# Performance work log

Hardware: AMD Instinct MI355X
Metric: run time of the kernel (lower is better)

## Reference

```python
import jax, jax.numpy as jnp
import numpy as np

WEIGHT_BITS = 8
INPUT_BITS = 8


def fake_quant(t, bits):
    """Per-tensor symmetric absmax fake quantization with straight-through estimator."""
    qmax = 2.0 ** (bits - 1) - 1.0  # e.g. 127 for 8 bits
    scale = jnp.maximum(jnp.max(jnp.abs(t)), 1e-8) / qmax
    q = jnp.round(t / scale) * scale
    return t + jax.lax.stop_gradient(q - t)


def setup_inputs() -> dict:
    key = jax.random.key(0)
    k0, k1, k2, k3 = jax.random.split(key, 4)
    d, f, n = 4096, 11008, 4096
    s_in = 1.0 / np.sqrt(d)
    s_ff = 1.0 / np.sqrt(f)
    return {
        "x": jax.random.normal(k0, (n, d), jnp.float32),
        "w1": jax.random.normal(k1, (f, d), jnp.float32) * s_in,  # fc1: embed -> ffn
        "w3": jax.random.normal(k2, (f, d), jnp.float32) * s_in,  # fc3: gate proj
        "w2": jax.random.normal(k3, (d, f), jnp.float32) * s_ff,  # fc2: ffn -> embed
    }


def reference(x, w1, w3, w2):
    # quantized fc3 -> silu gate
    xq = fake_quant(x, INPUT_BITS)
    gate = jax.nn.silu(jnp.einsum('nd,fd->nf', xq, fake_quant(w3, WEIGHT_BITS)))
    # quantized fc1, multiplied by gate (GLU)
    h = jnp.einsum('nd,fd->nf', xq, fake_quant(w1, WEIGHT_BITS)) * gate
    # subln=False -> no ffn_layernorm; dropout=0 (eval)
    hq = fake_quant(h, INPUT_BITS)
    out = jnp.einsum('nf,df->nd', hq, fake_quant(w2, WEIGHT_BITS))
    return out
```

## Files before the change

### kernel.cpp

```cpp
#include <hip/hip_runtime.h>
#include <hip/hip_bf16.h>

typedef __attribute__((ext_vector_type(4))) int int4v;

#define MFMA_I8(a, b, c) __builtin_amdgcn_mfma_i32_16x16x64_i8((a), (b), (c), 0, 0, 0)
#define GLDS16(g, l)                                                                        \
  __builtin_amdgcn_global_load_lds((const __attribute__((address_space(1))) void*)(g),      \
                                   (__attribute__((address_space(3))) void*)(l), 16, 0, 0)
#define SBAR() __builtin_amdgcn_s_barrier()
#define SCHED0() __builtin_amdgcn_sched_barrier(0)

static constexpr int NTOK = 4096;
static constexpr int DDIM = 4096;
static constexpr int FDIM = 11008;


__device__ __forceinline__ float wave_max64(float m) {
#pragma unroll
  for (int o = 32; o > 0; o >>= 1) m = fmaxf(m, __shfl_xor(m, o));
  return m;
}

__global__ void zero_slots(unsigned* s) {
  if (threadIdx.x < 16) s[threadIdx.x] = 0u;
}

__device__ __forceinline__ void absmax_body(const float* __restrict__ p, int n4,
                                            unsigned* __restrict__ slot) {
  float m = 0.f;
  const int stride = gridDim.x * blockDim.x;
  for (int i = blockIdx.x * blockDim.x + threadIdx.x; i < n4; i += stride) {
    float4 v = reinterpret_cast<const float4*>(p)[i];
    m = fmaxf(fmaxf(fabsf(v.x), fabsf(v.y)), fmaxf(fmaxf(fabsf(v.z), fabsf(v.w)), m));
  }
  m = wave_max64(m);
  __shared__ float wm[4];
  const int lane = threadIdx.x & 63, w = threadIdx.x >> 6;
  if (lane == 0) wm[w] = m;
  __syncthreads();
  if (threadIdx.x == 0) {
    m = fmaxf(fmaxf(wm[0], wm[1]), fmaxf(wm[2], wm[3]));
    atomicMax(slot, __float_as_uint(m));
  }
}

__global__ void absmax4(const float* x, const float* w1, const float* w3, const float* w2,
                        unsigned* slots, int n4x, int n4w) {
  const int seg = blockIdx.y;
  const float* p = (seg == 0) ? x : (seg == 1) ? w1 : (seg == 2) ? w3 : w2;
  absmax_body(p, seg == 0 ? n4x : n4w, slots + seg);
}

__device__ __forceinline__ void quant_body(const float* __restrict__ in,
                                           unsigned* __restrict__ out, int n4,
                                           const unsigned* __restrict__ slot) {
  const float s = fmaxf(__uint_as_float(*slot), 1e-8f) / 127.0f;
  const int stride = gridDim.x * blockDim.x;
  for (int i = blockIdx.x * blockDim.x + threadIdx.x; i < n4; i += stride) {
    float4 v = reinterpret_cast<const float4*>(in)[i];
    const int q0 = (int)rintf(v.x / s), q1 = (int)rintf(v.y / s);
    const int q2 = (int)rintf(v.z / s), q3 = (int)rintf(v.w / s);
    out[i] = (unsigned)(q0 & 255) | ((unsigned)(q1 & 255) << 8) |
             ((unsigned)(q2 & 255) << 16) | ((unsigned)(q3 & 255) << 24);
  }
}

__device__ __forceinline__ void quantW_frag_body(const float* __restrict__ in,
                                                 int4v* __restrict__ out,
                                                 const unsigned* __restrict__ slot) {
  const float s = fmaxf(__uint_as_float(*slot), 1e-8f) / 127.0f;
  const int total = FDIM * (DDIM / 16);
  const int stride = gridDim.x * blockDim.x;
  for (int u = blockIdx.x * blockDim.x + threadIdx.x; u < total; u += stride) {
    const int block = u >> 8;
    const int sidx = u & 255;
    const int fi = sidx >> 6;
    const int l = sidx & 63;
    const int p = block >> 5;
    const int kt = block & 31;
    const int f = p * 32 + (fi & 1) * 16 + (l & 15);
    const int k0 = kt * 128 + (fi >> 1) * 64 + (l >> 4) * 16;
    const float4* src = reinterpret_cast<const float4*>(in + (size_t)f * DDIM + k0);
    unsigned r[4];
#pragma unroll
    for (int j = 0; j < 4; ++j) {
      float4 v = src[j];
      const int q0 = (int)rintf(v.x / s), q1 = (int)rintf(v.y / s);
      const int q2 = (int)rintf(v.z / s), q3 = (int)rintf(v.w / s);
      r[j] = (unsigned)(q0 & 255) | ((unsigned)(q1 & 255) << 8) |
             ((unsigned)(q2 & 255) << 16) | ((unsigned)(q3 & 255) << 24);
    }
    out[u] = (int4v){(int)r[0], (int)r[1], (int)r[2], (int)r[3]};
  }
}

__global__ void quant4(const float* x, const float* w1, const float* w3, const float* w2,
                       unsigned* qx, unsigned* qw1, unsigned* qw3, unsigned* qw2,
                       const unsigned* slots, int n4x, int n4w) {
  const int seg = blockIdx.y;
  if (seg == 0) quant_body(x, qx, n4x, slots + 0);
  else if (seg == 1) quantW_frag_body(w1, (int4v*)qw1, slots + 1);
  else if (seg == 2) quantW_frag_body(w3, (int4v*)qw3, slots + 2);
  else quant_body(w2, qw2, n4w, slots + 3);
}

__global__ void quant_kernel(const float* __restrict__ in, unsigned* __restrict__ out,
                             int n4, const unsigned* __restrict__ slot) {
  quant_body(in, out, n4, slot);
}

__global__ __launch_bounds__(512, 2) void gemm_glu(
    const signed char* __restrict__ Aq, const signed char* __restrict__ B3f,
    const signed char* __restrict__ B1f, float* __restrict__ H,
    const unsigned* __restrict__ slots, unsigned* __restrict__ hslot) {
  constexpr int K = DDIM;
  constexpr int NT = K >> 7;
  __shared__ char lds[32768];

  const int t = threadIdx.x;
  const int l = t & 63;
  const int w = t >> 6;

  const int gx = gridDim.x, gy = gridDim.y;
  const int nwg = gx * gy;
  const int i0 = blockIdx.y * gx + blockIdx.x;
  const int cid = (i0 & 7) * (nwg >> 3) + (i0 >> 3);
  const int rowA0 = (cid % gy) << 7;
  const int colB0 = (cid / gy) << 8;

  const int rlA = t >> 3;
  const int glA = (t & 7) ^ (rlA & 7);
  const signed char* aP = Aq + (size_t)(rowA0 + rlA) * K + glA * 16;
  const size_t r64 = (size_t)64 * K;
  const int stW = w * 1024;

  const int p0 = (colB0 >> 5) + w;
  const signed char* w3b = B3f + (size_t)p0 * 32 * 4096 + l * 16;
  const signed char* w1b = B1f + (size_t)p0 * 32 * 4096 + l * 16;

#define STAGE_A(KT, BUF)                               \
  do {                                                 \
    const size_t kO_ = (size_t)(KT) * 128;             \
    GLDS16(aP + kO_, &lds[(BUF) + stW]);               \
    GLDS16(aP + r64 + kO_, &lds[(BUF) + 8192 + stW]);  \
  } while (0)

#define LDSF(BASE, R, G)                                                      \
  (*reinterpret_cast<const int4v*>(                                           \
      &lds[(BASE) + (R)*128 + (((G) ^ ((R)&7)) << 4)]))

  int4v acc3[8][2], acc1[8][2];
#pragma unroll
  for (int m = 0; m < 8; ++m)
#pragma unroll
    for (int n = 0; n < 2; ++n) {
      acc3[m][n] = (int4v){0, 0, 0, 0};
      acc1[m][n] = (int4v){0, 0, 0, 0};
    }

  const int lr = l & 15;
  const int cr = l >> 4;

  int4v b3k0[2], b3k1[2], b1k0[2], b1k1[2];

  STAGE_A(0, 0);
  {
    const signed char* p3_ = w3b;
    const signed char* p1_ = w1b;
    b3k0[0] = *(const int4v*)(p3_);
    b3k0[1] = *(const int4v*)(p3_ + 1024);
    b3k1[0] = *(const int4v*)(p3_ + 2048);
    b3k1[1] = *(const int4v*)(p3_ + 3072);
    b1k0[0] = *(const int4v*)(p1_);
    b1k0[1] = *(const int4v*)(p1_ + 1024);
    b1k1[0] = *(const int4v*)(p1_ + 2048);
    b1k1[1] = *(const int4v*)(p1_ + 3072);
  }

  for (int kt = 0; kt < NT; ++kt) {
    const int rb = (kt & 1) * 16384;
    const bool nx = (kt + 1 < NT);
    const signed char* p3n = w3b + (size_t)(kt + 1) * 4096;
    const signed char* p1n = w1b + (size_t)(kt + 1) * 4096;

    SCHED0();
    asm volatile("s_waitcnt vmcnt(8)" ::: "memory");
    SBAR();
    SCHED0();

    if (nx) STAGE_A(kt + 1, rb ^ 16384);

    int4v a_[8];
#pragma unroll
    for (int m = 0; m < 8; ++m) a_[m] = LDSF(rb, m * 16 + lr, cr);
    __builtin_amdgcn_s_setprio(1);
#pragma unroll
    for (int m = 0; m < 8; ++m) {
      acc3[m][0] = MFMA_I8(a_[m], b3k0[0], acc3[m][0]);
      acc3[m][1] = MFMA_I8(a_[m], b3k0[1], acc3[m][1]);
      acc1[m][0] = MFMA_I8(a_[m], b1k0[0], acc1[m][0]);
      acc1[m][1] = MFMA_I8(a_[m], b1k0[1], acc1[m][1]);
    }
    __builtin_amdgcn_s_setprio(0);

    if (nx) {
      b3k0[0] = *(const int4v*)(p3n);
      b3k0[1] = *(const int4v*)(p3n + 1024);
      b1k0[0] = *(const int4v*)(p1n);
      b1k0[1] = *(const int4v*)(p1n + 1024);
    }

#pragma unroll
    for (int m = 0; m < 8; ++m) a_[m] = LDSF(rb, m * 16 + lr, 4 + cr);
    __builtin_amdgcn_s_setprio(1);
#pragma unroll
    for (int m = 0; m < 8; ++m) {
      acc3[m][0] = MFMA_I8(a_[m], b3k1[0], acc3[m][0]);
      acc3[m][1] = MFMA_I8(a_[m], b3k1[1], acc3[m][1]);
      acc1[m][0] = MFMA_I8(a_[m], b1k1[0], acc1[m][0]);
      acc1[m][1] = MFMA_I8(a_[m], b1k1[1], acc1[m][1]);
    }
    __builtin_amdgcn_s_setprio(0);

    if (nx) {
      b3k1[0] = *(const int4v*)(p3n + 2048);
      b3k1[1] = *(const int4v*)(p3n + 3072);
      b1k1[0] = *(const int4v*)(p1n + 2048);
      b1k1[1] = *(const int4v*)(p1n + 3072);
    }
  }

  const float sx = fmaxf(__uint_as_float(slots[0]), 1e-8f) / 127.0f;
  const float sw1 = fmaxf(__uint_as_float(slots[1]), 1e-8f) / 127.0f;
  const float sw3 = fmaxf(__uint_as_float(slots[2]), 1e-8f) / 127.0f;
  const float s3 = sx * sw3, s1 = sx * sw1;
  const int crow0 = rowA0 + ((l >> 4) << 2);
  const int ccol0 = colB0 + w * 32 + lr;
  float hmax = 0.f;
#pragma unroll
  for (int m = 0; m < 8; ++m)
#pragma unroll
    for (int n = 0; n < 2; ++n)
#pragma unroll
      for (int j = 0; j < 4; ++j) {
        const int row = crow0 + m * 16 + j;
        const int col = ccol0 + n * 16;
        const float g = (float)acc3[m][n][j] * s3;
        const float gate = g / (1.f + expf(-g));
        const float h = (float)acc1[m][n][j] * s1 * gate;
        H[(size_t)row * FDIM + col] = h;
        hmax = fmaxf(hmax, fabsf(h));
      }
  hmax = wave_max64(hmax);
  if (l == 0) atomicMax(hslot, __float_as_uint(hmax));
#undef STAGE_A
#undef LDSF
}

__global__ __launch_bounds__(512, 2) void gemm_down(
    const signed char* __restrict__ Aq, const signed char* __restrict__ Bq,
    float* __restrict__ C, const unsigned* __restrict__ slots, int sA, int sB,
    int K, int ldc) {
  __shared__ char lds[131072];

  const int t = threadIdx.x;
  const int l = t & 63;
  const int w = t >> 6;
  const int wm = w >> 2;
  const int wn = w & 3;

  const int gx = gridDim.x, gy = gridDim.y;
  const int nwg = gx * gy;
  const int i0 = blockIdx.y * gx + blockIdx.x;
  const int cid = (i0 & 7) * (nwg >> 3) + (i0 >> 3);
  const int rowA0 = (cid % gy) << 8;
  const int colB0 = (cid / gy) << 8;

  const int rl = t >> 3;
  const int gl = (t & 7) ^ (rl & 7);
  const signed char* aP = Aq + (size_t)(rowA0 + rl) * K + gl * 16;
  const signed char* bP = Bq + (size_t)(colB0 + rl) * K + gl * 16;
  const size_t r64 = (size_t)64 * K;
  const int stW = w * 1024;

#define STAGE8(KO, BASE)                                             \
  do {                                                               \
    GLDS16(aP + (KO), &lds[(BASE) + stW]);                           \
    GLDS16(aP + r64 + (KO), &lds[(BASE) + 8192 + stW]);              \
    GLDS16(aP + 2 * r64 + (KO), &lds[(BASE) + 16384 + stW]);         \
    GLDS16(aP + 3 * r64 + (KO), &lds[(BASE) + 24576 + stW]);         \
    GLDS16(bP + (KO), &lds[(BASE) + 32768 + stW]);                   \
    GLDS16(bP + r64 + (KO), &lds[(BASE) + 40960 + stW]);             \
    GLDS16(bP + 2 * r64 + (KO), &lds[(BASE) + 49152 + stW]);         \
    GLDS16(bP + 3 * r64 + (KO), &lds[(BASE) + 57344 + stW]);         \
  } while (0)

#define LDSF(BASE, ROW, G)                                                    \
  (*reinterpret_cast<const int4v*>(                                           \
      &lds[(BASE) + (ROW)*128 + (((G) ^ ((ROW)&7)) << 4)]))

  int4v acc[8][4];
#pragma unroll
  for (int m = 0; m < 8; ++m)
#pragma unroll
    for (int n = 0; n < 4; ++n) acc[m][n] = (int4v){0, 0, 0, 0};

  const int NT = K >> 7;
  const int arow = wm * 128 + (l & 15);
  const int brow = wn * 64 + (l & 15);
  const int cr = l >> 4;

  STAGE8(0, 0);

  for (int kt = 0; kt < NT; ++kt) {
    const int rb = (kt & 1) * 65536;
    SCHED0();
    asm volatile("s_waitcnt vmcnt(0)" ::: "memory");
    SBAR();
    SCHED0();

    if (kt + 1 < NT) STAGE8((size_t)(kt + 1) * 128, rb ^ 65536);

#pragma unroll
    for (int kk = 0; kk < 2; ++kk) {
      int4v a[8], b[4];
#pragma unroll
      for (int m = 0; m < 8; ++m) a[m] = LDSF(rb, arow + m * 16, kk * 4 + cr);
#pragma unroll
      for (int n = 0; n < 4; ++n) b[n] = LDSF(rb + 32768, brow + n * 16, kk * 4 + cr);
      __builtin_amdgcn_s_setprio(1);
#pragma unroll
      for (int m = 0; m < 8; ++m)
#pragma unroll
        for (int n = 0; n < 4; ++n) acc[m][n] = MFMA_I8(a[m], b[n], acc[m][n]);
      __builtin_amdgcn_s_setprio(0);
    }
  }

  const float sa = fmaxf(__uint_as_float(slots[sA]), 1e-8f) / 127.0f;
  const float sb2 = fmaxf(__uint_as_float(slots[sB]), 1e-8f) / 127.0f;
  const float s = sa * sb2;
  const int crow0 = rowA0 + wm * 128 + ((l >> 4) << 2);
  const int ccol0 = colB0 + wn * 64 + (l & 15);
#pragma unroll
  for (int m = 0; m < 8; ++m)
#pragma unroll
    for (int n = 0; n < 4; ++n)
#pragma unroll
      for (int j = 0; j < 4; ++j) {
        const int row = crow0 + m * 16 + j;
        const int col = ccol0 + n * 16;
        C[(size_t)row * ldc + col] = (float)acc[m][n][j] * s;
      }
#undef STAGE8
#undef LDSF
}


extern "C" void kernel_launch(void* const* d_in, const int* in_sizes, int n_in,
                              void* d_out, int out_size, void* d_ws, size_t ws_size,
                              hipStream_t stream) {
  const float* x = (const float*)d_in[0];
  const float* w1 = (const float*)d_in[1];
  const float* w3 = (const float*)d_in[2];
  const float* w2 = (const float*)d_in[3];
  float* out = (float*)d_out;
  char* ws = (char*)d_ws;

  unsigned* slots = (unsigned*)ws;
  size_t off = 256;
  signed char* qx = (signed char*)(ws + off);
  off += (size_t)NTOK * DDIM;
  signed char* qw3 = (signed char*)(ws + off);
  off += (size_t)FDIM * DDIM;
  signed char* qw1 = (signed char*)(ws + off);
  off += (size_t)FDIM * DDIM;
  signed char* qw2 = (signed char*)(ws + off);
  off += (size_t)FDIM * DDIM;
  float* H = (float*)(ws + off);
  off += (size_t)NTOK * FDIM * 4;
  signed char* qh = (signed char*)(ws + off);
  off += (size_t)NTOK * FDIM;

  const int n4x = NTOK * DDIM / 4;
  const int n4w = FDIM * DDIM / 4;
  const int n4h = NTOK * FDIM / 4;

  zero_slots<<<1, 64, 0, stream>>>(slots);
  absmax4<<<dim3(512, 4), 256, 0, stream>>>(x, w1, w3, w2, slots, n4x, n4w);
  quant4<<<dim3(2048, 4), 256, 0, stream>>>(x, w1, w3, w2, (unsigned*)qx, (unsigned*)qw1,
                                            (unsigned*)qw3, (unsigned*)qw2, slots, n4x, n4w);

  const dim3 gGlu(FDIM / 256, NTOK / 128);
  gemm_glu<<<gGlu, 512, 0, stream>>>(qx, qw3, qw1, H, slots, slots + 4);
  quant_kernel<<<2048, 256, 0, stream>>>(H, (unsigned*)qh, n4h, slots + 4);
  const dim3 gDn(DDIM / 256, NTOK / 256);
  gemm_down<<<gDn, 512, 0, stream>>>(qh, qw2, out, slots, 4, 3, FDIM, DDIM);
}
```

Measured before the change: 887.2 us.

## Shrink GLU tiles and restructure down GEMM with pre-fragmented register-streamed weights

The down-projection weight w2 is now quantized straight into the MFMA fragment layout. gemm_down is rewritten to match gemm_glu: only the activation tile is staged through LDS (32KB), and B fragments stream from global memory into registers. Both GEMMs move to 256-thread blocks with 128x128 output tiles, giving more workgroups and, for gemm_down, a target of 3 blocks per CU. The trade-off is less data reuse per tile and more B traffic from global memory or L2, in exchange for lower LDS usage and higher occupancy.

```diff
diff --git a/kernel.cpp b/kernel.cpp
--- a/kernel.cpp
+++ b/kernel.cpp
@@ -67,20 +67,20 @@
 
 __device__ __forceinline__ void quantW_frag_body(const float* __restrict__ in,
                                                  int4v* __restrict__ out,
-                                                 const unsigned* __restrict__ slot) {
+                                                 const unsigned* __restrict__ slot,
+                                                 int K, int NKT, int total) {
   const float s = fmaxf(__uint_as_float(*slot), 1e-8f) / 127.0f;
-  const int total = FDIM * (DDIM / 16);
   const int stride = gridDim.x * blockDim.x;
   for (int u = blockIdx.x * blockDim.x + threadIdx.x; u < total; u += stride) {
     const int block = u >> 8;
     const int sidx = u & 255;
     const int fi = sidx >> 6;
     const int l = sidx & 63;
-    const int p = block >> 5;
-    const int kt = block & 31;
-    const int f = p * 32 + (fi & 1) * 16 + (l & 15);
+    const int p = block / NKT;
+    const int kt = block - p * NKT;
+    const int row = p * 32 + (fi & 1) * 16 + (l & 15);
     const int k0 = kt * 128 + (fi >> 1) * 64 + (l >> 4) * 16;
-    const float4* src = reinterpret_cast<const float4*>(in + (size_t)f * DDIM + k0);
+    const float4* src = reinterpret_cast<const float4*>(in + (size_t)row * K + k0);
     unsigned r[4];
 #pragma unroll
     for (int j = 0; j < 4; ++j) {
@@ -98,10 +98,11 @@
                        unsigned* qx, unsigned* qw1, unsigned* qw3, unsigned* qw2,
                        const unsigned* slots, int n4x, int n4w) {
   const int seg = blockIdx.y;
+  const int totW = FDIM * (DDIM / 16);
   if (seg == 0) quant_body(x, qx, n4x, slots + 0);
-  else if (seg == 1) quantW_frag_body(w1, (int4v*)qw1, slots + 1);
-  else if (seg == 2) quantW_frag_body(w3, (int4v*)qw3, slots + 2);
-  else quant_body(w2, qw2, n4w, slots + 3);
+  else if (seg == 1) quantW_frag_body(w1, (int4v*)qw1, slots + 1, DDIM, DDIM / 128, totW);
+  else if (seg == 2) quantW_frag_body(w3, (int4v*)qw3, slots + 2, DDIM, DDIM / 128, totW);
+  else quantW_frag_body(w2, (int4v*)qw2, slots + 3, FDIM, FDIM / 128, totW);
 }
 
 __global__ void quant_kernel(const float* __restrict__ in, unsigned* __restrict__ out,
@@ -109,7 +110,7 @@
   quant_body(in, out, n4, slot);
 }
 
-__global__ __launch_bounds__(512, 2) void gemm_glu(
+__global__ __launch_bounds__(256, 2) void gemm_glu(
     const signed char* __restrict__ Aq, const signed char* __restrict__ B3f,
     const signed char* __restrict__ B1f, float* __restrict__ H,
     const unsigned* __restrict__ slots, unsigned* __restrict__ hslot) {
@@ -126,23 +127,25 @@
   const int i0 = blockIdx.y * gx + blockIdx.x;
   const int cid = (i0 & 7) * (nwg >> 3) + (i0 >> 3);
   const int rowA0 = (cid % gy) << 7;
-  const int colB0 = (cid / gy) << 8;
+  const int colB0 = (cid / gy) << 7;
 
   const int rlA = t >> 3;
   const int glA = (t & 7) ^ (rlA & 7);
   const signed char* aP = Aq + (size_t)(rowA0 + rlA) * K + glA * 16;
-  const size_t r64 = (size_t)64 * K;
+  const size_t r32 = (size_t)32 * K;
   const int stW = w * 1024;
 
   const int p0 = (colB0 >> 5) + w;
   const signed char* w3b = B3f + (size_t)p0 * 32 * 4096 + l * 16;
   const signed char* w1b = B1f + (size_t)p0 * 32 * 4096 + l * 16;
 
-#define STAGE_A(KT, BUF)                               \
-  do {                                                 \
-    const size_t kO_ = (size_t)(KT) * 128;             \
-    GLDS16(aP + kO_, &lds[(BUF) + stW]);               \
-    GLDS16(aP + r64 + kO_, &lds[(BUF) + 8192 + stW]);  \
+#define STAGE_A(KT, BUF)                                   \
+  do {                                                     \
+    const size_t kO_ = (size_t)(KT) * 128;                 \
+    GLDS16(aP + kO_, &lds[(BUF) + stW]);                   \
+    GLDS16(aP + r32 + kO_, &lds[(BUF) + 4096 + stW]);      \
+    GLDS16(aP + 2 * r32 + kO_, &lds[(BUF) + 8192 + stW]);  \
+    GLDS16(aP + 3 * r32 + kO_, &lds[(BUF) + 12288 + stW]); \
   } while (0)
 
 #define LDSF(BASE, R, G)                                                      \
@@ -165,16 +168,14 @@
 
   STAGE_A(0, 0);
   {
-    const signed char* p3_ = w3b;
-    const signed char* p1_ = w1b;
-    b3k0[0] = *(const int4v*)(p3_);
-    b3k0[1] = *(const int4v*)(p3_ + 1024);
-    b3k1[0] = *(const int4v*)(p3_ + 2048);
-    b3k1[1] = *(const int4v*)(p3_ + 3072);
-    b1k0[0] = *(const int4v*)(p1_);
-    b1k0[1] = *(const int4v*)(p1_ + 1024);
-    b1k1[0] = *(const int4v*)(p1_ + 2048);
-    b1k1[1] = *(const int4v*)(p1_ + 3072);
+    b3k0[0] = *(const int4v*)(w3b);
+    b3k0[1] = *(const int4v*)(w3b + 1024);
+    b3k1[0] = *(const int4v*)(w3b + 2048);
+    b3k1[1] = *(const int4v*)(w3b + 3072);
+    b1k0[0] = *(const int4v*)(w1b);
+    b1k0[1] = *(const int4v*)(w1b + 1024);
+    b1k1[0] = *(const int4v*)(w1b + 2048);
+    b1k1[1] = *(const int4v*)(w1b + 3072);
   }
 
   for (int kt = 0; kt < NT; ++kt) {
@@ -257,102 +258,124 @@
 #undef LDSF
 }
 
-__global__ __launch_bounds__(512, 2) void gemm_down(
-    const signed char* __restrict__ Aq, const signed char* __restrict__ Bq,
-    float* __restrict__ C, const unsigned* __restrict__ slots, int sA, int sB,
-    int K, int ldc) {
-  __shared__ char lds[131072];
+__global__ __launch_bounds__(256, 3) void gemm_down(
+    const signed char* __restrict__ Aq, const signed char* __restrict__ B2f,
+    float* __restrict__ C, const unsigned* __restrict__ slots) {
+  constexpr int K = FDIM;
+  constexpr int NT = K >> 7;
+  constexpr int NKT = K >> 7;
+  __shared__ char lds[32768];
 
   const int t = threadIdx.x;
   const int l = t & 63;
   const int w = t >> 6;
-  const int wm = w >> 2;
-  const int wn = w & 3;
 
   const int gx = gridDim.x, gy = gridDim.y;
   const int nwg = gx * gy;
   const int i0 = blockIdx.y * gx + blockIdx.x;
   const int cid = (i0 & 7) * (nwg >> 3) + (i0 >> 3);
-  const int rowA0 = (cid % gy) << 8;
-  const int colB0 = (cid / gy) << 8;
-
-  const int rl = t >> 3;
-  const int gl = (t & 7) ^ (rl & 7);
-  const signed char* aP = Aq + (size_t)(rowA0 + rl) * K + gl * 16;
-  const signed char* bP = Bq + (size_t)(colB0 + rl) * K + gl * 16;
-  const size_t r64 = (size_t)64 * K;
+  const int rowA0 = (cid % gy) << 7;
+  const int colB0 = (cid / gy) << 7;
+
+  const int rlA = t >> 3;
+  const int glA = (t & 7) ^ (rlA & 7);
+  const signed char* aP = Aq + (size_t)(rowA0 + rlA) * K + glA * 16;
+  const size_t r32 = (size_t)32 * K;
   const int stW = w * 1024;
 
-#define STAGE8(KO, BASE)                                             \
-  do {                                                               \
-    GLDS16(aP + (KO), &lds[(BASE) + stW]);                           \
-    GLDS16(aP + r64 + (KO), &lds[(BASE) + 8192 + stW]);              \
-    GLDS16(aP + 2 * r64 + (KO), &lds[(BASE) + 16384 + stW]);         \
-    GLDS16(aP + 3 * r64 + (KO), &lds[(BASE) + 24576 + stW]);         \
-    GLDS16(bP + (KO), &lds[(BASE) + 32768 + stW]);                   \
-    GLDS16(bP + r64 + (KO), &lds[(BASE) + 40960 + stW]);             \
-    GLDS16(bP + 2 * r64 + (KO), &lds[(BASE) + 49152 + stW]);         \
-    GLDS16(bP + 3 * r64 + (KO), &lds[(BASE) + 57344 + stW]);         \
+  const int p0 = (colB0 >> 5) + w;
+  const signed char* w2b = B2f + (size_t)p0 * NKT * 4096 + l * 16;
+
+#define STAGE_A(KT, BUF)                                   \
+  do {                                                     \
+    const size_t kO_ = (size_t)(KT) * 128;                 \
+    GLDS16(aP + kO_, &lds[(BUF) + stW]);                   \
+    GLDS16(aP + r32 + kO_, &lds[(BUF) + 4096 + stW]);      \
+    GLDS16(aP + 2 * r32 + kO_, &lds[(BUF) + 8192 + stW]);  \
+    GLDS16(aP + 3 * r32 + kO_, &lds[(BUF) + 12288 + stW]); \
   } while (0)
 
-#define LDSF(BASE, ROW, G)                                                    \
+#define LDSF(BASE, R, G)                                                      \
   (*reinterpret_cast<const int4v*>(                                           \
-      &lds[(BASE) + (ROW)*128 + (((G) ^ ((ROW)&7)) << 4)]))
-
-  int4v acc[8][4];
+      &lds[(BASE) + (R)*128 + (((G) ^ ((R)&7)) << 4)]))
+
+  int4v acc[8][2];
 #pragma unroll
   for (int m = 0; m < 8; ++m)
 #pragma unroll
-    for (int n = 0; n < 4; ++n) acc[m][n] = (int4v){0, 0, 0, 0};
-
-  const int NT = K >> 7;
-  const int arow = wm * 128 + (l & 15);
-  const int brow = wn * 64 + (l & 15);
+    for (int n = 0; n < 2; ++n) acc[m][n] = (int4v){0, 0, 0, 0};
+
+  const int lr = l & 15;
   const int cr = l >> 4;
 
-  STAGE8(0, 0);
+  int4v bk0[2], bk1[2];
+
+  STAGE_A(0, 0);
+  bk0[0] = *(const int4v*)(w2b);
+  bk0[1] = *(const int4v*)(w2b + 1024);
+  bk1[0] = *(const int4v*)(w2b + 2048);
+  bk1[1] = *(const int4v*)(w2b + 3072);
 
   for (int kt = 0; kt < NT; ++kt) {
-    const int rb = (kt & 1) * 65536;
+    const int rb = (kt & 1) * 16384;
+    const bool nx = (kt + 1 < NT);
+    const signed char* pn = w2b + (size_t)(kt + 1) * 4096;
+
     SCHED0();
-    asm volatile("s_waitcnt vmcnt(0)" ::: "memory");
+    asm volatile("s_waitcnt vmcnt(4)" ::: "memory");
     SBAR();
     SCHED0();
 
-    if (kt + 1 < NT) STAGE8((size_t)(kt + 1) * 128, rb ^ 65536);
-
-#pragma unroll
-    for (int kk = 0; kk < 2; ++kk) {
-      int4v a[8], b[4];
-#pragma unroll
-      for (int m = 0; m < 8; ++m) a[m] = LDSF(rb, arow + m * 16, kk * 4 + cr);
-#pragma unroll
-      for (int n = 0; n < 4; ++n) b[n] = LDSF(rb + 32768, brow + n * 16, kk * 4 + cr);
-      __builtin_amdgcn_s_setprio(1);
-#pragma unroll
-      for (int m = 0; m < 8; ++m)
-#pragma unroll
-        for (int n = 0; n < 4; ++n) acc[m][n] = MFMA_I8(a[m], b[n], acc[m][n]);
-      __builtin_amdgcn_s_setprio(0);
-    }
-  }
-
-  const float sa = fmaxf(__uint_as_float(slots[sA]), 1e-8f) / 127.0f;
-  const float sb2 = fmaxf(__uint_as_float(slots[sB]), 1e-8f) / 127.0f;
-  const float s = sa * sb2;
-  const int crow0 = rowA0 + wm * 128 + ((l >> 4) << 2);
-  const int ccol0 = colB0 + wn * 64 + (l & 15);
+    if (nx) STAGE_A(kt + 1, rb ^ 16384);
+
+    int4v a_[8];
+#pragma unroll
+    for (int m = 0; m < 8; ++m) a_[m] = LDSF(rb, m * 16 + lr, cr);
+    __builtin_amdgcn_s_setprio(1);
+#pragma unroll
+    for (int m = 0; m < 8; ++m) {
+      acc[m][0] = MFMA_I8(a_[m], bk0[0], acc[m][0]);
+      acc[m][1] = MFMA_I8(a_[m], bk0[1], acc[m][1]);
+    }
+    __builtin_amdgcn_s_setprio(0);
+
+    if (nx) {
+      bk0[0] = *(const int4v*)(pn);
+      bk0[1] = *(const int4v*)(pn + 1024);
+    }
+
+#pragma unroll
+    for (int m = 0; m < 8; ++m) a_[m] = LDSF(rb, m * 16 + lr, 4 + cr);
+    __builtin_amdgcn_s_setprio(1);
+#pragma unroll
+    for (int m = 0; m < 8; ++m) {
+      acc[m][0] = MFMA_I8(a_[m], bk1[0], acc[m][0]);
+      acc[m][1] = MFMA_I8(a_[m], bk1[1], acc[m][1]);
+    }
+    __builtin_amdgcn_s_setprio(0);
+
+    if (nx) {
+      bk1[0] = *(const int4v*)(pn + 2048);
+      bk1[1] = *(const int4v*)(pn + 3072);
+    }
+  }
+
+  const float sa = fmaxf(__uint_as_float(slots[4]), 1e-8f) / 127.0f;
+  const float sb = fmaxf(__uint_as_float(slots[3]), 1e-8f) / 127.0f;
+  const float s = sa * sb;
+  const int crow0 = rowA0 + ((l >> 4) << 2);
+  const int ccol0 = colB0 + w * 32 + lr;
 #pragma unroll
   for (int m = 0; m < 8; ++m)
 #pragma unroll
-    for (int n = 0; n < 4; ++n)
+    for (int n = 0; n < 2; ++n)
 #pragma unroll
       for (int j = 0; j < 4; ++j) {
         const int row = crow0 + m * 16 + j;
         const int col = ccol0 + n * 16;
-        C[(size_t)row * ldc + col] = (float)acc[m][n][j] * s;
+        C[(size_t)row * DDIM + col] = (float)acc[m][n][j] * s;
       }
-#undef STAGE8
+#undef STAGE_A
 #undef LDSF
 }
 
@@ -391,9 +414,9 @@
   quant4<<<dim3(2048, 4), 256, 0, stream>>>(x, w1, w3, w2, (unsigned*)qx, (unsigned*)qw1,
                                             (unsigned*)qw3, (unsigned*)qw2, slots, n4x, n4w);
 
-  const dim3 gGlu(FDIM / 256, NTOK / 128);
-  gemm_glu<<<gGlu, 512, 0, stream>>>(qx, qw3, qw1, H, slots, slots + 4);
+  const dim3 gGlu(FDIM / 128, NTOK / 128);
+  gemm_glu<<<gGlu, 256, 0, stream>>>(qx, qw3, qw1, H, slots, slots + 4);
   quant_kernel<<<2048, 256, 0, stream>>>(H, (unsigned*)qh, n4h, slots + 4);
-  const dim3 gDn(DDIM / 256, NTOK / 256);
-  gemm_down<<<gDn, 512, 0, stream>>>(qh, qw2, out, slots, 4, 3, FDIM, DDIM);
-}
+  const dim3 gDn(DDIM / 128, NTOK / 128);
+  gemm_down<<<gDn, 256, 0, stream>>>(qh, qw2, out, slots);
+}
```

Measured after the change: 894.3 us. No clear change (+0.8%).
